# Kernel optimization log

Hardware: AMD Instinct MI355X
Metric: run time of the kernel (lower is better)

## Reference

```python
import jax, jax.numpy as jnp
import numpy as np

D = 768
HEADS = 8
DC = D // HEADS        # dim_conv = head_dim = 96
B = 2
T, Hs, Ws = 8, 28, 28  # thw_shape
N = T * Hs * Ws
SCALE = DC ** -0.5
EPS = 1e-5


def _dwconv3d(x, w, stride):
    # x: [N, C, T, H, W], w: [C, 1, 3, 3, 3] depthwise (groups=C), padding k//2=1
    return jax.lax.conv_general_dilated(
        x, w, window_strides=tuple(stride), padding=[(1, 1)] * 3,
        dimension_numbers=('NCDHW', 'OIDHW', 'NCDHW'),
        feature_group_count=x.shape[1])


def _ln(x, g, b):
    m = jnp.mean(x, axis=-1, keepdims=True)
    v = jnp.mean(jnp.square(x - m), axis=-1, keepdims=True)
    return (x - m) * jax.lax.rsqrt(v + EPS) * g + b


def _attention_pool(xh, w, g, b, thw, stride):
    # xh: [B, heads, L, dim_conv]; mirrors attention_pool (no cls token)
    Bb, Hh, L, Cc = xh.shape
    Tt, Hi, Wi = thw
    t = xh.reshape(Bb * Hh, Tt, Hi, Wi, Cc).transpose(0, 4, 1, 2, 3)  # [B*h, C, T, H, W]
    t = _dwconv3d(t, w, stride)
    To, Ho, Wo = t.shape[2], t.shape[3], t.shape[4]
    Lp = To * Ho * Wo
    t = t.reshape(Bb, Hh, Cc, Lp).transpose(0, 1, 3, 2)  # [B, h, Lp, C]
    t = _ln(t, g, b)
    return t, (To, Ho, Wo)


def setup_inputs() -> dict:
    key = jax.random.key(0)
    ks = jax.random.split(key, 10)
    std = 0.02
    inp = {
        'x': jax.random.normal(ks[0], (B, N, D), dtype=jnp.float32),
        'pool_q_w': jax.random.normal(ks[1], (DC, 1, 3, 3, 3), dtype=jnp.float32) * std,
        'pool_k_w': jax.random.normal(ks[2], (DC, 1, 3, 3, 3), dtype=jnp.float32) * std,
        'pool_v_w': jax.random.normal(ks[3], (DC, 1, 3, 3, 3), dtype=jnp.float32) * std,
        'norm_q_g': jnp.ones((DC,), jnp.float32), 'norm_q_b': jnp.zeros((DC,), jnp.float32),
        'norm_k_g': jnp.ones((DC,), jnp.float32), 'norm_k_b': jnp.zeros((DC,), jnp.float32),
        'norm_v_g': jnp.ones((DC,), jnp.float32), 'norm_v_b': jnp.zeros((DC,), jnp.float32),
        'lin_q_w': jax.random.normal(ks[4], (D, D), dtype=jnp.float32) * std,
        'lin_k_w': jax.random.normal(ks[5], (D, D), dtype=jnp.float32) * std,
        'lin_v_w': jax.random.normal(ks[6], (D, D), dtype=jnp.float32) * std,
        'proj_w': jax.random.normal(ks[7], (D, D), dtype=jnp.float32) * std,
        'proj_b': jnp.zeros((D,), jnp.float32),
        'thw_t': T, 'thw_h': Hs, 'thw_w': Ws,
    }
    return inp


def reference(x, pool_q_w, pool_k_w, pool_v_w,
              norm_q_g, norm_q_b, norm_k_g, norm_k_b, norm_v_g, norm_v_b,
              lin_q_w, lin_k_w, lin_v_w, proj_w, proj_b,
              thw_t, thw_h, thw_w):
    Bb, Nn, _ = x.shape
    thw = (thw_t, thw_h, thw_w)
    xh = x.reshape(Bb, Nn, HEADS, DC).transpose(0, 2, 1, 3)  # [B, h, N, dc]
    q, q_shape = _attention_pool(xh, pool_q_w, norm_q_g, norm_q_b, thw, (1, 1, 1))
    k, _ = _attention_pool(xh, pool_k_w, norm_k_g, norm_k_b, thw, (1, 2, 2))
    v, _ = _attention_pool(xh, pool_v_w, norm_v_g, norm_v_b, thw, (1, 2, 2))
    qN, kN = q.shape[2], k.shape[2]
    # back to [B, L, C] (pool_first): first forward, mem cache empty -> just q/k/v
    q = q.transpose(0, 2, 1, 3).reshape(Bb, qN, D)
    k = k.transpose(0, 2, 1, 3).reshape(Bb, kN, D)
    v = v.transpose(0, 2, 1, 3).reshape(Bb, kN, D)
    # linear projections (no bias), split heads
    q = (q @ lin_q_w.T).reshape(Bb, qN, HEADS, DC).transpose(0, 2, 1, 3)
    k = (k @ lin_k_w.T).reshape(Bb, kN, HEADS, DC).transpose(0, 2, 1, 3)
    v = (v @ lin_v_w.T).reshape(Bb, kN, HEADS, DC).transpose(0, 2, 1, 3)
    attn = jnp.einsum('bhqd,bhkd->bhqk', q * SCALE, k)
    attn = jax.nn.softmax(attn, axis=-1)
    out = jnp.einsum('bhqk,bhkd->bhqd', attn, v)
    out = out.transpose(0, 2, 1, 3).reshape(Bb, qN, D)
    out = out @ proj_w.T + proj_b
    return out
```

## Files before the change

### kernel.cpp

```cpp
#include <hip/hip_runtime.h>

#define DEV __device__ __forceinline__

typedef float f32x4 __attribute__((ext_vector_type(4)));
typedef __bf16 b16x8 __attribute__((ext_vector_type(8)));
typedef __bf16 b16x4 __attribute__((ext_vector_type(4)));
typedef __bf16 b16x2 __attribute__((ext_vector_type(2)));

DEV f32x4 mfma16(b16x8 a, b16x8 b, f32x4 c) {
  return __builtin_amdgcn_mfma_f32_16x16x32_bf16(a, b, c, 0, 0, 0);
}
DEV void gload_lds16(const __bf16* g, __bf16* l) {
  __builtin_amdgcn_global_load_lds((const __attribute__((address_space(1))) void*)g,
                                   (__attribute__((address_space(3))) void*)l, 16, 0, 0);
}

#define QN 6272
#define KN 1568
#define SCALE 0.10206207261596575f

DEV int vperm32(int kv) {
  return (kv < 16) ? ((kv >> 2) * 8 + (kv & 3)) : (((kv - 16) >> 2) * 8 + 4 + (kv & 3));
}

__global__ __launch_bounds__(256) void cast4(const float* __restrict__ s0, const float* __restrict__ s1,
                                             const float* __restrict__ s2, const float* __restrict__ s3,
                                             __bf16* __restrict__ d0, __bf16* __restrict__ d1,
                                             __bf16* __restrict__ d2, __bf16* __restrict__ d3) {
  int which = blockIdx.y;
  const float* s = which == 0 ? s0 : which == 1 ? s1 : which == 2 ? s2 : s3;
  __bf16* d = which == 0 ? d0 : which == 1 ? d1 : which == 2 ? d2 : d3;
  int i = (blockIdx.x * 256 + threadIdx.x) * 4;
  f32x4 v = *(const f32x4*)&s[i];
  b16x4 o;
  o[0] = (__bf16)v[0]; o[1] = (__bf16)v[1]; o[2] = (__bf16)v[2]; o[3] = (__bf16)v[3];
  *(b16x4*)&d[i] = o;
}

__global__ __launch_bounds__(64) void pool_ln(const float* __restrict__ x,
                                              const float* __restrict__ w,
                                              const float* __restrict__ gg,
                                              const float* __restrict__ bb,
                                              __bf16* __restrict__ out,
                                              int sh, int Ho, int Wo) {
  int h = blockIdx.y, b = blockIdx.z;
  int tid = threadIdx.x;
  bool act = tid < 48;
  int Lout = 8 * Ho * Wo, hw = Ho * Wo;

  float wr[54];
  float g0 = 0.f, g1 = 0.f, b0 = 0.f, b1 = 0.f;
  if (act) {
    #pragma unroll
    for (int i = 0; i < 27; ++i) { wr[i] = w[(2 * tid) * 27 + i]; wr[27 + i] = w[(2 * tid + 1) * 27 + i]; }
    g0 = gg[2 * tid]; g1 = gg[2 * tid + 1];
    b0 = bb[2 * tid]; b1 = bb[2 * tid + 1];
  } else {
    #pragma unroll
    for (int i = 0; i < 54; ++i) wr[i] = 0.f;
  }
  const float* xb = x + ((size_t)b * QN) * 768 + h * 96 + 2 * tid;

  for (int pp = 0; pp < 8; ++pp) {
    int l = blockIdx.x * 8 + pp;
    int t = l / hw;
    int rr = l - t * hw;
    int yo = rr / Wo, xo = rr - (rr / Wo) * Wo;
    int yc = yo * sh, xc = xo * sh;

    float a0 = 0.f, a1 = 0.f;
    if (act) {
      #pragma unroll
      for (int kt = 0; kt < 3; ++kt) {
        int it = t + kt - 1;
        if (it < 0 || it >= 8) continue;
        #pragma unroll
        for (int ky = 0; ky < 3; ++ky) {
          int iy = yc + ky - 1;
          if (iy < 0 || iy >= 28) continue;
          #pragma unroll
          for (int kx = 0; kx < 3; ++kx) {
            int ix = xc + kx - 1;
            if (ix < 0 || ix >= 28) continue;
            float2 v = *(const float2*)&xb[(size_t)(it * 784 + iy * 28 + ix) * 768];
            a0 += v.x * wr[kt * 9 + ky * 3 + kx];
            a1 += v.y * wr[27 + kt * 9 + ky * 3 + kx];
          }
        }
      }
    }
    float s = a0 + a1, s2 = a0 * a0 + a1 * a1;
    #pragma unroll
    for (int d = 1; d < 64; d <<= 1) { s += __shfl_xor(s, d); s2 += __shfl_xor(s2, d); }
    if (act) {
      float mean = s * (1.f / 96.f);
      float var = s2 * (1.f / 96.f) - mean * mean;
      float rstd = rsqrtf(var + 1e-5f);
      b16x2 yy;
      yy[0] = (__bf16)((a0 - mean) * rstd * g0 + b0);
      yy[1] = (__bf16)((a1 - mean) * rstd * g1 + b1);
      *(b16x2*)&out[((size_t)b * Lout + l) * 768 + h * 96 + 2 * tid] = yy;
    }
  }
}

template <int MODE>
DEV void gemm_core(const __bf16* __restrict__ A, const __bf16* __restrict__ W,
                   void* __restrict__ outp, const float* __restrict__ bias,
                   int M, float scale, int bx, int by, __bf16* As, __bf16* Bs) {
  int m0 = bx * 128, n0 = by * 128;
  int tid = threadIdx.x;
  int w = tid >> 6, lane = tid & 63;
  int wr = (w >> 1) * 64, wc = (w & 1) * 64;
  int rl = lane & 15, g8 = (lane >> 4) * 8;

  f32x4 acc[4][4] = {};

  auto stage = [&](int kt, int bsel) {
    #pragma unroll
    for (int ii = 0; ii < 2; ++ii) {
      int ch = tid + ii * 256;
      int row = ch >> 2, cc = ch & 3;
      int ar = m0 + row;
      ar = ar < M ? ar : M - 1;
      gload_lds16(&A[(size_t)ar * 768 + kt * 32 + cc * 8], &As[bsel * 4096 + ch * 8]);
      gload_lds16(&W[(size_t)(n0 + row) * 768 + kt * 32 + cc * 8], &Bs[bsel * 4096 + ch * 8]);
    }
  };

  stage(0, 0);
  __syncthreads();
  for (int kt = 0; kt < 24; ++kt) {
    if (kt < 23) stage(kt + 1, (kt + 1) & 1);
    const __bf16* as = &As[(kt & 1) * 4096];
    const __bf16* bs = &Bs[(kt & 1) * 4096];
    b16x8 af[4], bfr[4];
    #pragma unroll
    for (int i = 0; i < 4; ++i) af[i] = *(const b16x8*)&as[(wr + i * 16 + rl) * 32 + g8];
    #pragma unroll
    for (int j = 0; j < 4; ++j) bfr[j] = *(const b16x8*)&bs[(wc + j * 16 + rl) * 32 + g8];
    __builtin_amdgcn_s_setprio(1);
    #pragma unroll
    for (int i = 0; i < 4; ++i)
      #pragma unroll
      for (int j = 0; j < 4; ++j) acc[i][j] = mfma16(af[i], bfr[j], acc[i][j]);
    __builtin_amdgcn_s_setprio(0);
    __syncthreads();
  }

  int g4 = (lane >> 4) * 4;
  #pragma unroll
  for (int i = 0; i < 4; ++i) {
    #pragma unroll
    for (int j = 0; j < 4; ++j) {
      #pragma unroll
      for (int reg = 0; reg < 4; ++reg) {
        int r = m0 + wr + i * 16 + g4 + reg;
        int col = n0 + wc + j * 16 + rl;
        if (r < M) {
          float v = acc[i][j][reg] * scale;
          if constexpr (MODE == 0) {
            ((__bf16*)outp)[(size_t)r * 768 + col] = (__bf16)v;
          } else if constexpr (MODE == 1) {
            int bb2 = r >= KN ? 1 : 0;
            int jr = r - bb2 * KN;
            int jp = (jr & ~31) + vperm32(jr & 31);
            int hh = col / 96;
            int ccc = col - hh * 96;
            ((__bf16*)outp)[((size_t)(bb2 * 8 + hh) * 96 + ccc) * KN + jp] = (__bf16)v;
          } else {
            ((float*)outp)[(size_t)r * 768 + col] = v + bias[col];
          }
        }
      }
    }
  }
}

__global__ __launch_bounds__(256) void gemm_qkv(const __bf16* plq, const __bf16* plk, const __bf16* plv,
                                                const __bf16* wq, const __bf16* wk, const __bf16* wv,
                                                __bf16* qproj, __bf16* kproj, __bf16* vtr) {
  __shared__ __align__(16) __bf16 As[2 * 4096];
  __shared__ __align__(16) __bf16 Bs[2 * 4096];
  int bx = blockIdx.x, by = blockIdx.y;
  if (bx < 98)       gemm_core<0>(plq, wq, qproj, nullptr, 2 * QN, SCALE, bx, by, As, Bs);
  else if (bx < 123) gemm_core<0>(plk, wk, kproj, nullptr, 2 * KN, 1.f, bx - 98, by, As, Bs);
  else               gemm_core<1>(plv, wv, vtr, nullptr, 2 * KN, 1.f, bx - 123, by, As, Bs);
}

__global__ __launch_bounds__(256) void gemm_proj(const __bf16* A, const __bf16* W,
                                                 float* outp, const float* bias) {
  __shared__ __align__(16) __bf16 As[2 * 4096];
  __shared__ __align__(16) __bf16 Bs[2 * 4096];
  gemm_core<2>(A, W, outp, bias, 2 * QN, 1.f, blockIdx.x, blockIdx.y, As, Bs);
}

__global__ __launch_bounds__(256) void attn_kernel(const __bf16* __restrict__ qp,
                                                   const __bf16* __restrict__ kp,
                                                   const __bf16* __restrict__ vt,
                                                   __bf16* __restrict__ ao) {
  __shared__ __align__(16) __bf16 kls[2][32 * 96];
  __shared__ __align__(16) __bf16 vls[2][96 * 32];

  int h = blockIdx.y, b = blockIdx.z;
  int tid = threadIdx.x, w = tid >> 6, lane = tid & 63;
  int rl = lane & 15, g = lane >> 4, g8 = g * 8;
  int q0 = blockIdx.x * 128 + w * 32;

  b16x8 qf[2][3];
  #pragma unroll
  for (int qt = 0; qt < 2; ++qt)
    #pragma unroll
    for (int ks = 0; ks < 3; ++ks)
      qf[qt][ks] = *(const b16x8*)&qp[((size_t)(b * QN + q0 + qt * 16 + rl)) * 768 + h * 96 + ks * 32 + g8];

  f32x4 o[2][6] = {};
  float lsum[2] = {0.f, 0.f};

  const __bf16* kbase = kp + (size_t)(b * KN) * 768 + h * 96;
  const __bf16* vbase = vt + ((size_t)(b * 8 + h) * 96) * KN;

  auto stage = [&](int st, int bsel) {
    int j0 = st * 32;
    #pragma unroll
    for (int i = 0; i < 3; ++i) {
      int ca = i * 256 + tid;
      if (ca < 384) {
        int row = ca / 12, cc = ca - (ca / 12) * 12;
        gload_lds16(&kbase[(size_t)(j0 + row) * 768 + cc * 8], &kls[bsel][ca * 8]);
      } else {
        int cv = ca - 384;
        int rv = cv >> 2, s = cv & 3;
        gload_lds16(&vbase[(size_t)rv * KN + j0 + s * 8], &vls[bsel][cv * 8]);
      }
    }
  };

  stage(0, 0);
  __syncthreads();

  for (int st = 0; st < 49; ++st) {
    if (st < 48) stage(st + 1, (st + 1) & 1);
    int bsel = st & 1;

    b16x8 kf[2][3];
    #pragma unroll
    for (int kt = 0; kt < 2; ++kt)
      #pragma unroll
      for (int ks = 0; ks < 3; ++ks)
        kf[kt][ks] = *(const b16x8*)&kls[bsel][(kt * 16 + rl) * 96 + ks * 32 + g8];
    f32x4 s[2][2] = {};
    __builtin_amdgcn_s_setprio(1);
    #pragma unroll
    for (int qt = 0; qt < 2; ++qt)
      #pragma unroll
      for (int kt = 0; kt < 2; ++kt)
        #pragma unroll
        for (int ks = 0; ks < 3; ++ks) s[qt][kt] = mfma16(kf[kt][ks], qf[qt][ks], s[qt][kt]);
    __builtin_amdgcn_s_setprio(0);

    b16x8 pf[2];
    #pragma unroll
    for (int qt = 0; qt < 2; ++qt) {
      float e0[4], e1[4];
      #pragma unroll
      for (int r = 0; r < 4; ++r) { e0[r] = __expf(s[qt][0][r]); e1[r] = __expf(s[qt][1][r]); }
      lsum[qt] += e0[0] + e0[1] + e0[2] + e0[3] + e1[0] + e1[1] + e1[2] + e1[3];
      #pragma unroll
      for (int r = 0; r < 4; ++r) { pf[qt][r] = (__bf16)e0[r]; pf[qt][4 + r] = (__bf16)e1[r]; }
    }

    b16x8 vf[6];
    #pragma unroll
    for (int cv = 0; cv < 6; ++cv) vf[cv] = *(const b16x8*)&vls[bsel][(cv * 16 + rl) * 32 + g8];
    __builtin_amdgcn_s_setprio(1);
    #pragma unroll
    for (int qt = 0; qt < 2; ++qt)
      #pragma unroll
      for (int cv = 0; cv < 6; ++cv) o[qt][cv] = mfma16(pf[qt], vf[cv], o[qt][cv]);
    __builtin_amdgcn_s_setprio(0);

    __syncthreads();
  }

  #pragma unroll
  for (int qt = 0; qt < 2; ++qt) {
    float red = lsum[qt];
    red += __shfl_xor(red, 16);
    red += __shfl_xor(red, 32);
    float inv[4];
    #pragma unroll
    for (int reg = 0; reg < 4; ++reg) inv[reg] = 1.f / __shfl(red, 4 * g + reg);
    #pragma unroll
    for (int cv = 0; cv < 6; ++cv)
      #pragma unroll
      for (int reg = 0; reg < 4; ++reg) {
        int row = q0 + qt * 16 + 4 * g + reg;
        int col = cv * 16 + rl;
        ao[((size_t)(b * QN + row)) * 768 + h * 96 + col] = (__bf16)(o[qt][cv][reg] * inv[reg]);
      }
  }
}

extern "C" void kernel_launch(void* const* d_in, const int* in_sizes, int n_in,
                              void* d_out, int out_size, void* d_ws, size_t ws_size,
                              hipStream_t stream) {
  const float* x   = (const float*)d_in[0];
  const float* pqw = (const float*)d_in[1];
  const float* pkw = (const float*)d_in[2];
  const float* pvw = (const float*)d_in[3];
  const float* nqg = (const float*)d_in[4];
  const float* nqb = (const float*)d_in[5];
  const float* nkg = (const float*)d_in[6];
  const float* nkb = (const float*)d_in[7];
  const float* nvg = (const float*)d_in[8];
  const float* nvb = (const float*)d_in[9];
  const float* lqw = (const float*)d_in[10];
  const float* lkw = (const float*)d_in[11];
  const float* lvw = (const float*)d_in[12];
  const float* pw  = (const float*)d_in[13];
  const float* pb  = (const float*)d_in[14];

  char* p = (char*)d_ws;
  auto carve = [&](size_t bytes) {
    char* r = p;
    p += (bytes + 255) & ~(size_t)255;
    return r;
  };
  const size_t WB = 589824 * 2;
  __bf16* wq = (__bf16*)carve(WB);
  __bf16* wk = (__bf16*)carve(WB);
  __bf16* wv = (__bf16*)carve(WB);
  __bf16* wp = (__bf16*)carve(WB);
  __bf16* plq   = (__bf16*)carve((size_t)2 * QN * 768 * 2);
  __bf16* plk   = (__bf16*)carve((size_t)2 * KN * 768 * 2);
  __bf16* plv   = (__bf16*)carve((size_t)2 * KN * 768 * 2);
  __bf16* qproj = (__bf16*)carve((size_t)2 * QN * 768 * 2);
  __bf16* kproj = (__bf16*)carve((size_t)2 * KN * 768 * 2);
  __bf16* vtr   = (__bf16*)carve((size_t)16 * 96 * KN * 2);
  __bf16* ao    = plq;

  cast4<<<dim3(576, 4), 256, 0, stream>>>(lqw, lkw, lvw, pw, wq, wk, wv, wp);

  pool_ln<<<dim3(784, 8, 2), 64, 0, stream>>>(x, pqw, nqg, nqb, plq, 1, 28, 28);
  pool_ln<<<dim3(196, 8, 2), 64, 0, stream>>>(x, pkw, nkg, nkb, plk, 2, 14, 14);
  pool_ln<<<dim3(196, 8, 2), 64, 0, stream>>>(x, pvw, nvg, nvb, plv, 2, 14, 14);

  gemm_qkv<<<dim3(148, 6), 256, 0, stream>>>(plq, plk, plv, wq, wk, wv, qproj, kproj, vtr);

  attn_kernel<<<dim3(49, 8, 2), 256, 0, stream>>>(qproj, kproj, vtr, ao);

  gemm_proj<<<dim3(98, 6), 256, 0, stream>>>(ao, wp, (float*)d_out, pb);
}
```

Measured before the change: 610.0 us.

## Fuse q/k/v pooling+LayerNorm into one kernel and XCD-swizzle block mapping

Replaces the three separate pool_ln launches with a single pool3 kernel in which each thread handles one channel and computes the q, k and v depthwise convolutions from the same input loads. The k and v outputs are written only at even (y,x) positions, which reproduces the stride-2 pooling, and the LayerNorm reduction now spans two waves through shared memory. This removes the repeated reads of x done by the separate k/v passes. The attention kernel and pool3 also remap linear block ids with an XCD swizzle so that blocks sharing a (b,h) land on the same chiplet for L2 locality. The cost is a __syncthreads per position and scalar rather than float2 loads.

```diff
diff --git a/kernel.cpp b/kernel.cpp
--- a/kernel.cpp
+++ b/kernel.cpp
@@ -5,7 +5,6 @@
 typedef float f32x4 __attribute__((ext_vector_type(4)));
 typedef __bf16 b16x8 __attribute__((ext_vector_type(8)));
 typedef __bf16 b16x4 __attribute__((ext_vector_type(4)));
-typedef __bf16 b16x2 __attribute__((ext_vector_type(2)));
 
 DEV f32x4 mfma16(b16x8 a, b16x8 b, f32x4 c) {
   return __builtin_amdgcn_mfma_f32_16x16x32_bf16(a, b, c, 0, 0, 0);
@@ -13,6 +12,10 @@
 DEV void gload_lds16(const __bf16* g, __bf16* l) {
   __builtin_amdgcn_global_load_lds((const __attribute__((address_space(1))) void*)g,
                                    (__attribute__((address_space(3))) void*)l, 16, 0, 0);
+}
+
+DEV int xcd_swizzle(int lin, int nb) {
+  return (lin & 7) * (nb >> 3) + (lin >> 3);
 }
 
 #define QN 6272
@@ -37,70 +40,98 @@
   *(b16x4*)&d[i] = o;
 }
 
-__global__ __launch_bounds__(64) void pool_ln(const float* __restrict__ x,
-                                              const float* __restrict__ w,
-                                              const float* __restrict__ gg,
-                                              const float* __restrict__ bb,
-                                              __bf16* __restrict__ out,
-                                              int sh, int Ho, int Wo) {
-  int h = blockIdx.y, b = blockIdx.z;
-  int tid = threadIdx.x;
-  bool act = tid < 48;
-  int Lout = 8 * Ho * Wo, hw = Ho * Wo;
-
-  float wr[54];
-  float g0 = 0.f, g1 = 0.f, b0 = 0.f, b1 = 0.f;
-  if (act) {
-    #pragma unroll
-    for (int i = 0; i < 27; ++i) { wr[i] = w[(2 * tid) * 27 + i]; wr[27 + i] = w[(2 * tid + 1) * 27 + i]; }
-    g0 = gg[2 * tid]; g1 = gg[2 * tid + 1];
-    b0 = bb[2 * tid]; b1 = bb[2 * tid + 1];
-  } else {
-    #pragma unroll
-    for (int i = 0; i < 54; ++i) wr[i] = 0.f;
-  }
-  const float* xb = x + ((size_t)b * QN) * 768 + h * 96 + 2 * tid;
+__global__ __launch_bounds__(128) void pool3(const float* __restrict__ x,
+                                             const float* __restrict__ wqp,
+                                             const float* __restrict__ wkp,
+                                             const float* __restrict__ wvp,
+                                             const float* __restrict__ gq, const float* __restrict__ bq,
+                                             const float* __restrict__ gk, const float* __restrict__ bk,
+                                             const float* __restrict__ gv, const float* __restrict__ bv,
+                                             __bf16* __restrict__ plq,
+                                             __bf16* __restrict__ plk,
+                                             __bf16* __restrict__ plv) {
+  int work = xcd_swizzle(blockIdx.x, 12544);
+  int posblk = work % 784;
+  int bh = work / 784;
+  int h = bh & 7, b = bh >> 3;
+
+  int tid = threadIdx.x, wvi = tid >> 6;
+  bool act = tid < 96;
+  int c = act ? tid : 95;
+
+  float wq[27], wk[27], wvv[27];
+  #pragma unroll
+  for (int i = 0; i < 27; ++i) {
+    wq[i] = wqp[c * 27 + i]; wk[i] = wkp[c * 27 + i]; wvv[i] = wvp[c * 27 + i];
+  }
+  float gq_ = gq[c], bq_ = bq[c], gk_ = gk[c], bk_ = bk[c], gv_ = gv[c], bv_ = bv[c];
+
+  __shared__ float red[2][6];
+  const float* xb = x + ((size_t)b * QN) * 768 + h * 96 + c;
 
   for (int pp = 0; pp < 8; ++pp) {
-    int l = blockIdx.x * 8 + pp;
-    int t = l / hw;
-    int rr = l - t * hw;
-    int yo = rr / Wo, xo = rr - (rr / Wo) * Wo;
-    int yc = yo * sh, xc = xo * sh;
-
-    float a0 = 0.f, a1 = 0.f;
+    int l = posblk * 8 + pp;
+    int t = l / 784;
+    int rr = l - t * 784;
+    int yo = rr / 28, xo = rr - (rr / 28) * 28;
+    bool kvpos = ((yo | xo) & 1) == 0;
+
+    float aq = 0.f, ak = 0.f, av = 0.f;
+    #pragma unroll
+    for (int kt = 0; kt < 3; ++kt) {
+      int it = t + kt - 1;
+      if (it < 0 || it >= 8) continue;
+      #pragma unroll
+      for (int ky = 0; ky < 3; ++ky) {
+        int iy = yo + ky - 1;
+        if (iy < 0 || iy >= 28) continue;
+        #pragma unroll
+        for (int kx = 0; kx < 3; ++kx) {
+          int ix = xo + kx - 1;
+          if (ix < 0 || ix >= 28) continue;
+          float v = xb[(size_t)(it * 784 + iy * 28 + ix) * 768];
+          int wi = kt * 9 + ky * 3 + kx;
+          aq += v * wq[wi]; ak += v * wk[wi]; av += v * wvv[wi];
+        }
+      }
+    }
+
+    float zq = act ? aq : 0.f, zk = act ? ak : 0.f, zv = act ? av : 0.f;
+    float sq = zq, q2 = zq * zq, sk = zk, k2 = zk * zk, sv = zv, v2 = zv * zv;
+    if (kvpos) {
+      #pragma unroll
+      for (int d = 1; d < 64; d <<= 1) {
+        sq += __shfl_xor(sq, d); q2 += __shfl_xor(q2, d);
+        sk += __shfl_xor(sk, d); k2 += __shfl_xor(k2, d);
+        sv += __shfl_xor(sv, d); v2 += __shfl_xor(v2, d);
+      }
+    } else {
+      #pragma unroll
+      for (int d = 1; d < 64; d <<= 1) { sq += __shfl_xor(sq, d); q2 += __shfl_xor(q2, d); }
+    }
+    if ((tid & 63) == 0) {
+      red[wvi][0] = sq; red[wvi][1] = q2; red[wvi][2] = sk;
+      red[wvi][3] = k2; red[wvi][4] = sv; red[wvi][5] = v2;
+    }
+    __syncthreads();
     if (act) {
-      #pragma unroll
-      for (int kt = 0; kt < 3; ++kt) {
-        int it = t + kt - 1;
-        if (it < 0 || it >= 8) continue;
-        #pragma unroll
-        for (int ky = 0; ky < 3; ++ky) {
-          int iy = yc + ky - 1;
-          if (iy < 0 || iy >= 28) continue;
-          #pragma unroll
-          for (int kx = 0; kx < 3; ++kx) {
-            int ix = xc + kx - 1;
-            if (ix < 0 || ix >= 28) continue;
-            float2 v = *(const float2*)&xb[(size_t)(it * 784 + iy * 28 + ix) * 768];
-            a0 += v.x * wr[kt * 9 + ky * 3 + kx];
-            a1 += v.y * wr[27 + kt * 9 + ky * 3 + kx];
-          }
-        }
-      }
-    }
-    float s = a0 + a1, s2 = a0 * a0 + a1 * a1;
-    #pragma unroll
-    for (int d = 1; d < 64; d <<= 1) { s += __shfl_xor(s, d); s2 += __shfl_xor(s2, d); }
-    if (act) {
-      float mean = s * (1.f / 96.f);
-      float var = s2 * (1.f / 96.f) - mean * mean;
-      float rstd = rsqrtf(var + 1e-5f);
-      b16x2 yy;
-      yy[0] = (__bf16)((a0 - mean) * rstd * g0 + b0);
-      yy[1] = (__bf16)((a1 - mean) * rstd * g1 + b1);
-      *(b16x2*)&out[((size_t)b * Lout + l) * 768 + h * 96 + 2 * tid] = yy;
-    }
+      float Sq = red[0][0] + red[1][0], Q2 = red[0][1] + red[1][1];
+      float mq = Sq * (1.f / 96.f);
+      float rq = rsqrtf(Q2 * (1.f / 96.f) - mq * mq + 1e-5f);
+      plq[((size_t)b * QN + l) * 768 + h * 96 + c] = (__bf16)((aq - mq) * rq * gq_ + bq_);
+      if (kvpos) {
+        int lkv = t * 196 + (yo >> 1) * 14 + (xo >> 1);
+        float Sk = red[0][2] + red[1][2], K2 = red[0][3] + red[1][3];
+        float Sv = red[0][4] + red[1][4], V2 = red[0][5] + red[1][5];
+        float mk = Sk * (1.f / 96.f);
+        float rk = rsqrtf(K2 * (1.f / 96.f) - mk * mk + 1e-5f);
+        float mv = Sv * (1.f / 96.f);
+        float rv = rsqrtf(V2 * (1.f / 96.f) - mv * mv + 1e-5f);
+        plk[((size_t)b * KN + lkv) * 768 + h * 96 + c] = (__bf16)((ak - mk) * rk * gk_ + bk_);
+        plv[((size_t)b * KN + lkv) * 768 + h * 96 + c] = (__bf16)((av - mv) * rv * gv_ + bv_);
+      }
+    }
+    __syncthreads();
   }
 }
 
@@ -202,10 +233,14 @@
   __shared__ __align__(16) __bf16 kls[2][32 * 96];
   __shared__ __align__(16) __bf16 vls[2][96 * 32];
 
-  int h = blockIdx.y, b = blockIdx.z;
+  int work = xcd_swizzle(blockIdx.x, 784);
+  int qtile = work % 49;
+  int bh = work / 49;
+  int h = bh & 7, b = bh >> 3;
+
   int tid = threadIdx.x, w = tid >> 6, lane = tid & 63;
   int rl = lane & 15, g = lane >> 4, g8 = g * 8;
-  int q0 = blockIdx.x * 128 + w * 32;
+  int q0 = qtile * 128 + w * 32;
 
   b16x8 qf[2][3];
   #pragma unroll
@@ -342,13 +377,12 @@
 
   cast4<<<dim3(576, 4), 256, 0, stream>>>(lqw, lkw, lvw, pw, wq, wk, wv, wp);
 
-  pool_ln<<<dim3(784, 8, 2), 64, 0, stream>>>(x, pqw, nqg, nqb, plq, 1, 28, 28);
-  pool_ln<<<dim3(196, 8, 2), 64, 0, stream>>>(x, pkw, nkg, nkb, plk, 2, 14, 14);
-  pool_ln<<<dim3(196, 8, 2), 64, 0, stream>>>(x, pvw, nvg, nvb, plv, 2, 14, 14);
+  pool3<<<12544, 128, 0, stream>>>(x, pqw, pkw, pvw, nqg, nqb, nkg, nkb, nvg, nvb,
+                                   plq, plk, plv);
 
   gemm_qkv<<<dim3(148, 6), 256, 0, stream>>>(plq, plk, plv, wq, wk, wv, qproj, kproj, vtr);
 
-  attn_kernel<<<dim3(49, 8, 2), 256, 0, stream>>>(qproj, kproj, vtr, ao);
+  attn_kernel<<<784, 256, 0, stream>>>(qproj, kproj, vtr, ao);
 
   gemm_proj<<<dim3(98, 6), 256, 0, stream>>>(ao, wp, (float*)d_out, pb);
 }
```

After: 521.3 us. 14.6% less time.
